# Optimization experiments

Measured on AMD Instinct MI355X. Metric: run time of the kernel, lower is better.

The kernel has to match this reference:

```python
import jax, jax.numpy as jnp
import numpy as np


def _min_gru_layer(h_in, Wz, bz, Wh, bh):
    # h_in: [B, T, D_in]; gates/candidate via two GEMMs
    z = jax.nn.sigmoid(jnp.einsum('btd,dh->bth', h_in, Wz) + bz)  # [B,T,H]
    h_tilde = jnp.einsum('btd,dh->bth', h_in, Wh) + bh            # [B,T,H]
    # Recurrence h_t = a_t * h_{t-1} + b_t with a_t = 1-z_t, b_t = z_t*h_tilde.
    # h_0 = 0 (frozen zeros param in the torch module), so the associative
    # scan over (a, b) directly yields h_t for t = 1..T.
    a = 1.0 - z
    b = z * h_tilde

    def combine(c1, c2):
        a1, b1 = c1
        a2, b2 = c2
        return a1 * a2, a2 * b1 + b2

    _, h = jax.lax.associative_scan(combine, (a, b), axis=1)
    return h


def setup_inputs() -> dict:
    key = jax.random.key(0)
    ks = jax.random.split(key, 8)
    B, T, Din, H, Dout = 8, 4096, 512, 1024, 512
    s_in = 1.0 / np.sqrt(Din)
    s_h = 1.0 / np.sqrt(H)
    return {
        'x':   jax.random.normal(ks[0], (B, T, Din), dtype=jnp.float32),
        'Wz0': jax.random.normal(ks[1], (Din, H), dtype=jnp.float32) * s_in,
        'bz0': jnp.zeros((H,), dtype=jnp.float32),
        'Wh0': jax.random.normal(ks[2], (Din, H), dtype=jnp.float32) * s_in,
        'bh0': jnp.zeros((H,), dtype=jnp.float32),
        'Wz1': jax.random.normal(ks[3], (H, H), dtype=jnp.float32) * s_h,
        'bz1': jnp.zeros((H,), dtype=jnp.float32),
        'Wh1': jax.random.normal(ks[4], (H, H), dtype=jnp.float32) * s_h,
        'bh1': jnp.zeros((H,), dtype=jnp.float32),
        'Wfc': jax.random.normal(ks[5], (H, Dout), dtype=jnp.float32) * s_h,
        'bfc': jnp.zeros((Dout,), dtype=jnp.float32),
    }


def reference(x, Wz0, bz0, Wh0, bh0, Wz1, bz1, Wh1, bh1, Wfc, bfc):
    h = _min_gru_layer(x, Wz0, bz0, Wh0, bh0)   # layer 0
    h = _min_gru_layer(h, Wz1, bz1, Wh1, bh1)   # layer 1
    return jnp.einsum('bth,ho->bto', h, Wfc) + bfc
```

## Files before the change

kernel.cpp:

```cpp
#include <hip/hip_runtime.h>

typedef __attribute__((ext_vector_type(4))) float fv4;
typedef __attribute__((ext_vector_type(8))) _Float16 hv8;
typedef __attribute__((ext_vector_type(4))) _Float16 hv4;
typedef __attribute__((ext_vector_type(2))) _Float16 hv2;

__device__ __forceinline__ void gload16(const void* g, void* l) {
  __builtin_amdgcn_global_load_lds(
      (const __attribute__((address_space(1))) unsigned int*)g,
      (__attribute__((address_space(3))) unsigned int*)l, 16, 0, 0);
}

struct GemmCore {
  const _Float16 *ap0, *bp0;
  size_t half;
  _Float16 *ldsA0, *ldsA1, *ldsB0, *ldsB1;
  const _Float16 *fa0, *fa1, *fb0, *fb1;
  int wave;

  __device__ __forceinline__ void init(const _Float16* A, const _Float16* Bt,
                                       _Float16* lds, int m0, int n0, int K,
                                       int tid) {
    wave = tid >> 6;
    const int lane = tid & 63;
    const int wm = (wave >> 1), wn = (wave & 1);
    const int quad = lane >> 4, r = lane & 15;
    ldsA0 = lds;         ldsA1 = lds + 4096;
    ldsB0 = lds + 8192;  ldsB1 = lds + 12288;
    const int cg = (tid & 3) ^ ((tid >> 3) & 3);
    ap0 = A  + (size_t)(m0 + (tid >> 2)) * K + cg * 8;
    bp0 = Bt + (size_t)(n0 + (tid >> 2)) * K + cg * 8;
    half = (size_t)64 * K;
    const int sq = quad ^ ((r >> 1) & 3);
    fa0 = ldsA0 + (wm * 64 + r) * 32 + sq * 8;
    fa1 = ldsA1 + (wm * 64 + r) * 32 + sq * 8;
    fb0 = ldsB0 + (wn * 64 + r) * 32 + sq * 8;
    fb1 = ldsB1 + (wn * 64 + r) * 32 + sq * 8;
  }

  __device__ __forceinline__ void run(fv4 acc[4][4], int K) {
    const int kiters = K >> 6;
    for (int kk = 0; kk < kiters; ++kk) {
      gload16(ap0,             ldsA0 + wave * 512);
      gload16(ap0 + half,      ldsA0 + wave * 512 + 2048);
      gload16(ap0 + 32,        ldsA1 + wave * 512);
      gload16(ap0 + half + 32, ldsA1 + wave * 512 + 2048);
      gload16(bp0,             ldsB0 + wave * 512);
      gload16(bp0 + half,      ldsB0 + wave * 512 + 2048);
      gload16(bp0 + 32,        ldsB1 + wave * 512);
      gload16(bp0 + half + 32, ldsB1 + wave * 512 + 2048);
      ap0 += 64; bp0 += 64;
      __syncthreads();

      hv8 av[4], bv[4];
#pragma unroll
      for (int t = 0; t < 4; ++t) {
        av[t] = *(const hv8*)(fa0 + t * 512);
        bv[t] = *(const hv8*)(fb0 + t * 512);
      }
#pragma unroll
      for (int tm = 0; tm < 4; ++tm)
#pragma unroll
        for (int tn = 0; tn < 4; ++tn)
          acc[tm][tn] = __builtin_amdgcn_mfma_f32_16x16x32_f16(av[tm], bv[tn],
                                                               acc[tm][tn], 0, 0, 0);
#pragma unroll
      for (int t = 0; t < 4; ++t) {
        av[t] = *(const hv8*)(fa1 + t * 512);
        bv[t] = *(const hv8*)(fb1 + t * 512);
      }
#pragma unroll
      for (int tm = 0; tm < 4; ++tm)
#pragma unroll
        for (int tn = 0; tn < 4; ++tn)
          acc[tm][tn] = __builtin_amdgcn_mfma_f32_16x16x32_f16(av[tm], bv[tn],
                                                               acc[tm][tn], 0, 0, 0);
      __syncthreads();
    }
  }
};

__global__ __launch_bounds__(256)
void gemm_gate(const _Float16* __restrict__ A, const _Float16* __restrict__ Btf,
               _Float16* __restrict__ zh2,
               const float* __restrict__ bz, const float* __restrict__ bh,
               int K) {
  __shared__ _Float16 lds[4 * 128 * 32];
  const int tid  = threadIdx.x;
  const int lane = tid & 63;
  const int wave = tid >> 6;
  const int wm = wave >> 1, wn = wave & 1;
  const int quad = lane >> 4, r = lane & 15;
  const int m0 = blockIdx.y * 128;
  const int n0 = blockIdx.x * 128;

  GemmCore core;
  core.init(A, Btf, lds, m0, n0, K, tid);
  fv4 acc[4][4] = {};
  core.run(acc, K);

  const int jb   = (n0 + wn * 64) >> 1;
  const int row0 = m0 + wm * 64 + quad * 4;
#pragma unroll
  for (int tn = 0; tn < 2; ++tn) {
    const int j = jb + tn * 16 + r;
    const float bzv = bz[j];
    const float bhv = bh[j];
#pragma unroll
    for (int tm = 0; tm < 4; ++tm) {
#pragma unroll
      for (int r2 = 0; r2 < 4; ++r2) {
        const float zpre = acc[tm][tn][r2] + bzv;
        const float hpre = acc[tm][tn + 2][r2] + bhv;
        const float z = 1.0f / (1.0f + __expf(-zpre));
        hv2 ab = {(_Float16)(1.0f - z), (_Float16)(z * hpre)};
        *(hv2*)(zh2 + ((size_t)(row0 + tm * 16 + r2) * 1024 + j) * 2) = ab;
      }
    }
  }
}

__global__ __launch_bounds__(256)
void gemm_f16_bt(const _Float16* __restrict__ A, const _Float16* __restrict__ Bt,
                 float* __restrict__ C, const float* __restrict__ bias,
                 int N, int K) {
  __shared__ _Float16 lds[4 * 128 * 32];
  const int tid  = threadIdx.x;
  const int lane = tid & 63;
  const int wave = tid >> 6;
  const int wm = wave >> 1, wn = wave & 1;
  const int quad = lane >> 4, r = lane & 15;
  const int m0 = blockIdx.y * 128;
  const int n0 = blockIdx.x * 128;

  GemmCore core;
  core.init(A, Bt, lds, m0, n0, K, tid);
  fv4 acc[4][4] = {};
  core.run(acc, K);

  const int col0 = n0 + wn * 64 + r;
  const int row0 = m0 + wm * 64 + quad * 4;
#pragma unroll
  for (int tn = 0; tn < 4; ++tn) {
    const int col = col0 + tn * 16;
    const float bs = bias[col];
#pragma unroll
    for (int tm = 0; tm < 4; ++tm) {
#pragma unroll
      for (int r2 = 0; r2 < 4; ++r2) {
        C[(size_t)(row0 + tm * 16 + r2) * N + col] = acc[tm][tn][r2] + bs;
      }
    }
  }
}

__global__ void cvt_f16(const float* __restrict__ x, _Float16* __restrict__ y) {
  size_t i = ((size_t)blockIdx.x * 256 + threadIdx.x) * 4;
  fv4 v = *(const fv4*)(x + i);
  *(hv4*)(y + i) = __builtin_convertvector(v, hv4);
}

__global__ void transpose_cvt(const float* __restrict__ W, _Float16* __restrict__ Wt,
                              int K, int N, int mult, int off) {
  __shared__ float tile[32][33];
  const int tx = threadIdx.x, ty = threadIdx.y;
  const int n  = blockIdx.x * 32 + tx;
  const int kb = blockIdx.y * 32;
  for (int i = ty; i < 32; i += 8)
    tile[i][tx] = W[(size_t)(kb + i) * N + n];
  __syncthreads();
  const int k = kb + tx;
  for (int i = ty; i < 32; i += 8)
    Wt[(size_t)(blockIdx.x * mult + off + i) * K + k] = (_Float16)tile[tx][i];
}

__global__ void scan_phaseA(const _Float16* __restrict__ zh2,
                            float* __restrict__ cA, float* __restrict__ cB) {
  const int idx = blockIdx.x * 256 + threadIdx.x;
  const int h  = (idx & 255) * 4;
  const int c  = (idx >> 8) & 63;
  const int bb = idx >> 14;
  const size_t base = ((size_t)(bb * 4096 + c * 64) * 1024 + h) * 2;
  fv4 Aa = {1.0f, 1.0f, 1.0f, 1.0f};
  fv4 Bv = {0.0f, 0.0f, 0.0f, 0.0f};
#pragma unroll 4
  for (int t = 0; t < 64; ++t) {
    hv8 v = *(const hv8*)(zh2 + base + (size_t)t * 2048);
    fv4 av = __builtin_convertvector(__builtin_shufflevector(v, v, 0, 2, 4, 6), fv4);
    fv4 bv = __builtin_convertvector(__builtin_shufflevector(v, v, 1, 3, 5, 7), fv4);
    Aa = Aa * av;
    Bv = av * Bv + bv;
  }
  const size_t o = (size_t)(bb * 64 + c) * 1024 + h;
  *(fv4*)(cA + o) = Aa;
  *(fv4*)(cB + o) = Bv;
}

__global__ void scan_phaseB(const float* __restrict__ cA, const float* __restrict__ cB,
                            float* __restrict__ hcy) {
  const int gtid = blockIdx.x * 256 + threadIdx.x;
  const int lane = gtid & 63;
  const int wid  = gtid >> 6;
  const int h  = (wid & 255) * 4;
  const int bb = wid >> 8;
  const size_t o = (size_t)(bb * 64 + lane) * 1024 + h;
  fv4 Aa = *(const fv4*)(cA + o);
  fv4 Bv = *(const fv4*)(cB + o);
#pragma unroll
  for (int d = 1; d < 64; d <<= 1) {
    fv4 Ap, Bp;
#pragma unroll
    for (int k = 0; k < 4; ++k) {
      Ap[k] = __shfl_up(Aa[k], d, 64);
      Bp[k] = __shfl_up(Bv[k], d, 64);
    }
    if (lane >= d) {
      Bv = Aa * Bp + Bv;
      Aa = Ap * Aa;
    }
  }
  fv4 hc;
#pragma unroll
  for (int k = 0; k < 4; ++k) hc[k] = __shfl_up(Bv[k], 1, 64);
  if (lane == 0) { hc.x = 0.f; hc.y = 0.f; hc.z = 0.f; hc.w = 0.f; }
  *(fv4*)(hcy + o) = hc;
}

__global__ void scan_phaseC(const _Float16* __restrict__ zh2,
                            const float* __restrict__ hcy,
                            _Float16* __restrict__ hout) {
  const int idx = blockIdx.x * 256 + threadIdx.x;
  const int h  = (idx & 255) * 4;
  const int c  = (idx >> 8) & 63;
  const int bb = idx >> 14;
  const size_t base = ((size_t)(bb * 4096 + c * 64) * 1024 + h) * 2;
  const size_t ob   = (size_t)(bb * 4096 + c * 64) * 1024 + h;
  const size_t o    = (size_t)(bb * 64 + c) * 1024 + h;
  fv4 hc = *(const fv4*)(hcy + o);
#pragma unroll 4
  for (int t = 0; t < 64; ++t) {
    hv8 v = *(const hv8*)(zh2 + base + (size_t)t * 2048);
    fv4 av = __builtin_convertvector(__builtin_shufflevector(v, v, 0, 2, 4, 6), fv4);
    fv4 bv = __builtin_convertvector(__builtin_shufflevector(v, v, 1, 3, 5, 7), fv4);
    hc = av * hc + bv;
    *(hv4*)(hout + ob + (size_t)t * 1024) = __builtin_convertvector(hc, hv4);
  }
}

extern "C" void kernel_launch(void* const* d_in, const int* in_sizes, int n_in,
                              void* d_out, int out_size, void* d_ws, size_t ws_size,
                              hipStream_t stream) {
  const float* x   = (const float*)d_in[0];
  const float* Wz0 = (const float*)d_in[1];
  const float* bz0 = (const float*)d_in[2];
  const float* Wh0 = (const float*)d_in[3];
  const float* bh0 = (const float*)d_in[4];
  const float* Wz1 = (const float*)d_in[5];
  const float* bz1 = (const float*)d_in[6];
  const float* Wh1 = (const float*)d_in[7];
  const float* bh1 = (const float*)d_in[8];
  const float* Wfc = (const float*)d_in[9];
  const float* bfc = (const float*)d_in[10];

  const int Mrows = 32768;
  const int H = 1024, Din = 512, Dout = 512;

  char* w = (char*)d_ws;
  _Float16* zh2   = (_Float16*)w; w += (size_t)Mrows * 2 * H * 2;
  _Float16* hx    = (_Float16*)w; w += (size_t)Mrows * H * 2;
  _Float16* Wzh0t = (_Float16*)w; w += (size_t)2 * H * Din * 2;
  _Float16* Wzh1t = (_Float16*)w; w += (size_t)2 * H * H * 2;
  _Float16* Wft   = (_Float16*)w; w += (size_t)Dout * H * 2;
  float*    cA    = (float*)w;    w += (size_t)8 * 64 * H * 4;
  float*    cB    = (float*)w;    w += (size_t)8 * 64 * H * 4;
  float*    hcy   = (float*)w;    w += (size_t)8 * 64 * H * 4;
  _Float16* Xb    = hx;

  cvt_f16<<<Mrows * Din / 1024, 256, 0, stream>>>(x, Xb);
  transpose_cvt<<<dim3(H / 32, Din / 32), dim3(32, 8), 0, stream>>>(Wz0, Wzh0t, Din, H, 64, 0);
  transpose_cvt<<<dim3(H / 32, Din / 32), dim3(32, 8), 0, stream>>>(Wh0, Wzh0t, Din, H, 64, 32);
  transpose_cvt<<<dim3(H / 32, H / 32),   dim3(32, 8), 0, stream>>>(Wz1, Wzh1t, H, H, 64, 0);
  transpose_cvt<<<dim3(H / 32, H / 32),   dim3(32, 8), 0, stream>>>(Wh1, Wzh1t, H, H, 64, 32);
  transpose_cvt<<<dim3(Dout / 32, H / 32), dim3(32, 8), 0, stream>>>(Wfc, Wft, H, Dout, 32, 0);

  const dim3 gG(2 * H / 128, Mrows / 128);

  gemm_gate<<<gG, 256, 0, stream>>>(Xb, Wzh0t, zh2, bz0, bh0, Din);
  scan_phaseA<<<512, 256, 0, stream>>>(zh2, cA, cB);
  scan_phaseB<<<512, 256, 0, stream>>>(cA, cB, hcy);
  scan_phaseC<<<512, 256, 0, stream>>>(zh2, hcy, hx);

  gemm_gate<<<gG, 256, 0, stream>>>(hx, Wzh1t, zh2, bz1, bh1, H);
  scan_phaseA<<<512, 256, 0, stream>>>(zh2, cA, cB);
  scan_phaseB<<<512, 256, 0, stream>>>(cA, cB, hcy);
  scan_phaseC<<<512, 256, 0, stream>>>(zh2, hcy, hx);

  const dim3 gF(Dout / 128, Mrows / 128);
  gemm_f16_bt<<<gF, 256, 0, stream>>>(hx, Wft, (float*)d_out, bfc, Dout, H);
}
```

Baseline: 598.2 us.

## Fuse scan chunk reduction into gate GEMM epilogue and add XCD-aware tile mapping

The gate GEMM epilogue now reduces each 64-row chunk into scan carry pairs (A,B), using in-register products across the 4 rows, shuffles across quads and a serial combine across tm. These are written directly to cA/cB, so the separate scan_phaseA kernel and its re-read of zh2 are gone. The GEMMs also switch to a 1D grid whose block index is remapped so that blocks landing on the same XCD share M tiles, which should improve L2 reuse. The cost is extra epilogue work and shuffles in the GEMM, and the fused reduction depends on each wave's 64-row span lining up exactly with the scan chunk size.

```diff
diff --git a/kernel.cpp b/kernel.cpp
--- a/kernel.cpp
+++ b/kernel.cpp
@@ -80,19 +80,28 @@
   }
 };
 
+__device__ __forceinline__ void xcd_map(int bid, int ntl2, int mt_per_x,
+                                        int& m0, int& n0) {
+  const int xcd = bid & 7;
+  const int k2  = bid >> 3;
+  m0 = (xcd * mt_per_x + (k2 >> ntl2)) * 128;
+  n0 = (k2 & ((1 << ntl2) - 1)) * 128;
+}
+
 __global__ __launch_bounds__(256)
 void gemm_gate(const _Float16* __restrict__ A, const _Float16* __restrict__ Btf,
                _Float16* __restrict__ zh2,
+               float* __restrict__ cA, float* __restrict__ cB,
                const float* __restrict__ bz, const float* __restrict__ bh,
-               int K) {
+               int K, int ntl2, int mt_per_x) {
   __shared__ _Float16 lds[4 * 128 * 32];
   const int tid  = threadIdx.x;
   const int lane = tid & 63;
   const int wave = tid >> 6;
   const int wm = wave >> 1, wn = wave & 1;
   const int quad = lane >> 4, r = lane & 15;
-  const int m0 = blockIdx.y * 128;
-  const int n0 = blockIdx.x * 128;
+  int m0, n0;
+  xcd_map(blockIdx.x, ntl2, mt_per_x, m0, n0);
 
   GemmCore core;
   core.init(A, Btf, lds, m0, n0, K, tid);
@@ -101,21 +110,48 @@
 
   const int jb   = (n0 + wn * 64) >> 1;
   const int row0 = m0 + wm * 64 + quad * 4;
+  const int cidx = (m0 >> 6) + wm;
 #pragma unroll
   for (int tn = 0; tn < 2; ++tn) {
     const int j = jb + tn * 16 + r;
     const float bzv = bz[j];
     const float bhv = bh[j];
+    float qA[4], qB[4];
 #pragma unroll
     for (int tm = 0; tm < 4; ++tm) {
+      float sA = 1.0f, sB = 0.0f;
 #pragma unroll
       for (int r2 = 0; r2 < 4; ++r2) {
         const float zpre = acc[tm][tn][r2] + bzv;
         const float hpre = acc[tm][tn + 2][r2] + bhv;
         const float z = 1.0f / (1.0f + __expf(-zpre));
-        hv2 ab = {(_Float16)(1.0f - z), (_Float16)(z * hpre)};
+        const _Float16 a16 = (_Float16)(1.0f - z);
+        const _Float16 b16 = (_Float16)(z * hpre);
+        hv2 ab = {a16, b16};
         *(hv2*)(zh2 + ((size_t)(row0 + tm * 16 + r2) * 1024 + j) * 2) = ab;
+        const float af = (float)a16, bf = (float)b16;
+        sB = af * sB + bf;
+        sA = sA * af;
       }
+      qA[tm] = sA; qB[tm] = sB;
+    }
+#pragma unroll
+    for (int tm = 0; tm < 4; ++tm) {
+      float Av = qA[tm], Bv = qB[tm];
+      float Ap = __shfl_up(Av, 16, 64);
+      float Bp = __shfl_up(Bv, 16, 64);
+      if (quad >= 1) { Bv = Av * Bp + Bv; Av = Ap * Av; }
+      Ap = __shfl_up(Av, 32, 64);
+      Bp = __shfl_up(Bv, 32, 64);
+      if (quad >= 2) { Bv = Av * Bp + Bv; Av = Ap * Av; }
+      qA[tm] = Av; qB[tm] = Bv;
+    }
+    if (quad == 3) {
+      float CA = 1.0f, CB = 0.0f;
+#pragma unroll
+      for (int tm = 0; tm < 4; ++tm) { CB = qA[tm] * CB + qB[tm]; CA *= qA[tm]; }
+      cA[(size_t)cidx * 1024 + j] = CA;
+      cB[(size_t)cidx * 1024 + j] = CB;
     }
   }
 }
@@ -123,15 +159,15 @@
 __global__ __launch_bounds__(256)
 void gemm_f16_bt(const _Float16* __restrict__ A, const _Float16* __restrict__ Bt,
                  float* __restrict__ C, const float* __restrict__ bias,
-                 int N, int K) {
+                 int N, int K, int ntl2, int mt_per_x) {
   __shared__ _Float16 lds[4 * 128 * 32];
   const int tid  = threadIdx.x;
   const int lane = tid & 63;
   const int wave = tid >> 6;
   const int wm = wave >> 1, wn = wave & 1;
   const int quad = lane >> 4, r = lane & 15;
-  const int m0 = blockIdx.y * 128;
-  const int n0 = blockIdx.x * 128;
+  int m0, n0;
+  xcd_map(blockIdx.x, ntl2, mt_per_x, m0, n0);
 
   GemmCore core;
   core.init(A, Bt, lds, m0, n0, K, tid);
@@ -172,28 +208,6 @@
   const int k = kb + tx;
   for (int i = ty; i < 32; i += 8)
     Wt[(size_t)(blockIdx.x * mult + off + i) * K + k] = (_Float16)tile[tx][i];
-}
-
-__global__ void scan_phaseA(const _Float16* __restrict__ zh2,
-                            float* __restrict__ cA, float* __restrict__ cB) {
-  const int idx = blockIdx.x * 256 + threadIdx.x;
-  const int h  = (idx & 255) * 4;
-  const int c  = (idx >> 8) & 63;
-  const int bb = idx >> 14;
-  const size_t base = ((size_t)(bb * 4096 + c * 64) * 1024 + h) * 2;
-  fv4 Aa = {1.0f, 1.0f, 1.0f, 1.0f};
-  fv4 Bv = {0.0f, 0.0f, 0.0f, 0.0f};
-#pragma unroll 4
-  for (int t = 0; t < 64; ++t) {
-    hv8 v = *(const hv8*)(zh2 + base + (size_t)t * 2048);
-    fv4 av = __builtin_convertvector(__builtin_shufflevector(v, v, 0, 2, 4, 6), fv4);
-    fv4 bv = __builtin_convertvector(__builtin_shufflevector(v, v, 1, 3, 5, 7), fv4);
-    Aa = Aa * av;
-    Bv = av * Bv + bv;
-  }
-  const size_t o = (size_t)(bb * 64 + c) * 1024 + h;
-  *(fv4*)(cA + o) = Aa;
-  *(fv4*)(cB + o) = Bv;
 }
 
 __global__ void scan_phaseB(const float* __restrict__ cA, const float* __restrict__ cB,
@@ -283,18 +297,13 @@
   transpose_cvt<<<dim3(H / 32, H / 32),   dim3(32, 8), 0, stream>>>(Wh1, Wzh1t, H, H, 64, 32);
   transpose_cvt<<<dim3(Dout / 32, H / 32), dim3(32, 8), 0, stream>>>(Wfc, Wft, H, Dout, 32, 0);
 
-  const dim3 gG(2 * H / 128, Mrows / 128);
-
-  gemm_gate<<<gG, 256, 0, stream>>>(Xb, Wzh0t, zh2, bz0, bh0, Din);
-  scan_phaseA<<<512, 256, 0, stream>>>(zh2, cA, cB);
+  gemm_gate<<<4096, 256, 0, stream>>>(Xb, Wzh0t, zh2, cA, cB, bz0, bh0, Din, 4, 32);
   scan_phaseB<<<512, 256, 0, stream>>>(cA, cB, hcy);
   scan_phaseC<<<512, 256, 0, stream>>>(zh2, hcy, hx);
 
-  gemm_gate<<<gG, 256, 0, stream>>>(hx, Wzh1t, zh2, bz1, bh1, H);
-  scan_phaseA<<<512, 256, 0, stream>>>(zh2, cA, cB);
+  gemm_gate<<<4096, 256, 0, stream>>>(hx, Wzh1t, zh2, cA, cB, bz1, bh1, H, 4, 32);
   scan_phaseB<<<512, 256, 0, stream>>>(cA, cB, hcy);
   scan_phaseC<<<512, 256, 0, stream>>>(zh2, hcy, hx);
 
-  const dim3 gF(Dout / 128, Mrows / 128);
-  gemm_f16_bt<<<gF, 256, 0, stream>>>(hx, Wft, (float*)d_out, bfc, Dout, H);
-}
+  gemm_f16_bt<<<1024, 256, 0, stream>>>(hx, Wft, (float*)d_out, bfc, Dout, H, 2, 32);
+}
```

After: 558.0 us. 1.07x faster.
